# Optimization experiments

Hardware: AMD Instinct MI355X
Metric: run time of the kernel (lower is better)

## Reference

```python
import jax, jax.numpy as jnp
import numpy as np

IOU_THRESHOLD = 0.2


def setup_inputs() -> dict:
    key = jax.random.key(0)
    k1, k2, k3 = jax.random.split(key, 3)
    S, Q, X, Y, Z = 3, 64, 128, 128, 32
    C = 21  # 20 semantic classes + no-object
    voxel_logits = jax.random.normal(k1, (S, Q, X, Y, Z), dtype=jnp.float32)
    query_logits = jax.random.normal(k2, (S, 1, Q, C), dtype=jnp.float32)
    sem_prob_dense = jax.random.uniform(k3, (C, X, Y, Z), dtype=jnp.float32)
    return {"voxel_logits": voxel_logits, "query_logits": query_logits,
            "sem_prob_dense": sem_prob_dense}


def reference(voxel_logits, query_logits, sem_prob_dense):
    # voxel_logits: [S, Q, X, Y, Z], query_logits: [S, B, Q, C],
    # sem_prob_dense: [C_sem, X, Y, Z]
    S, Q, X, Y, Z = voxel_logits.shape
    N = X * Y * Z
    voxel_probs = jax.nn.sigmoid(voxel_logits).reshape(S, Q, N)   # MinkowskiSigmoid
    query_probs = jax.nn.softmax(query_logits, axis=-1)           # [S, B, Q, C]

    anchor_v = voxel_probs[0]   # [Q, N]
    anchor_q = query_probs[0]   # [B, Q, C]
    ious = []
    for i in range(1, S):  # small fixed loop over subnets
        aux_v = voxel_probs[i]
        # hard masks for IoU matching (find_matching_indices_v2)
        ma = (anchor_v > 0.5).astype(jnp.float32)  # [Q, N]
        mb = (aux_v > 0.5).astype(jnp.float32)     # [Q, N]
        inter = jnp.einsum('qn,pn->qp', ma, mb)    # [Q, Q]
        union = ma.sum(1)[:, None] + mb.sum(1)[None, :] - inter
        iou = inter / jnp.maximum(union, 1.0)
        aux_idx = jnp.argmax(iou, axis=1)          # best aux query per anchor
        iou_a = jnp.max(iou, axis=1)               # [Q]
        matched = iou_a > IOU_THRESHOLD
        # running-average merge of matched queries, weight i : 1
        merged_q = (anchor_q * i + query_probs[i][:, aux_idx, :]) / (i + 1)
        anchor_q = jnp.where(matched[None, :, None], merged_q, anchor_q)
        merged_v = (anchor_v * i + aux_v[aux_idx]) / (i + 1)
        anchor_v = jnp.where(matched[:, None], merged_v, anchor_v)
        ious.append(iou_a)

    iou_mean = jnp.stack(ious, axis=0).mean(0)     # [Q]
    keep = (iou_mean > IOU_THRESHOLD).astype(anchor_v.dtype)
    # mask out voxels whose ensemble semantic class is empty (class 0)
    sem_class = jnp.argmax(sem_prob_dense, axis=0)           # [X, Y, Z]
    occ = (sem_class != 0).astype(anchor_v.dtype).reshape(N)
    out = anchor_v * keep[:, None] * occ[None, :]
    return out.reshape(Q, X, Y, Z)
```

## Files before the change

### kernel.cpp

```cpp
#include <hip/hip_runtime.h>
#include <hip/hip_fp16.h>

#define NVOX 524288
#define NV4  131072
#define WPR  8192
#define QN   64
#define SN   3
#define CN   21

typedef unsigned long long u64;
typedef float vfloat4 __attribute__((ext_vector_type(4)));

struct __align__(8) half4 { __half2 lo, hi; };

__device__ __forceinline__ float fast_sigmoid(float x) {
    return __builtin_amdgcn_rcpf(1.0f + __expf(-x));
}

__device__ __forceinline__ void nt_store4(float4 v, float4* p) {
    vfloat4 nv = {v.x, v.y, v.z, v.w};
    __builtin_nontemporal_store(nv, (vfloat4*)p);
}

__global__ __launch_bounds__(256) void mask_rowsum_kernel(
    const float4* __restrict__ logits4, u64* __restrict__ B,
    unsigned int* __restrict__ part) {
    int r = blockIdx.x >> 3, c = blockIdx.x & 7;
    int tid = threadIdx.x, lane = tid & 63, wave = tid >> 6;
    const float4* row = logits4 + (size_t)r * NV4;
    int base = c * (NV4 / 8);
    int pcnt = 0;
#pragma unroll 2
    for (int it = 0; it < 64; ++it) {
        int idx = base + it * 256 + tid;
        float4 v = row[idx];
        int nib = (v.x > 0.f ? 1 : 0) | (v.y > 0.f ? 2 : 0) |
                  (v.z > 0.f ? 4 : 0) | (v.w > 0.f ? 8 : 0);
        pcnt += __popc(nib);
        u64 b0 = __ballot(nib & 1);
        u64 b1 = __ballot(nib & 2);
        u64 b2 = __ballot(nib & 4);
        u64 b3 = __ballot(nib & 8);
        if (lane == 0) {
            int seg = idx >> 6;
            ulonglong2* dst = (ulonglong2*)&B[(size_t)r * WPR + (size_t)seg * 4];
            dst[0] = make_ulonglong2(b0, b1);
            dst[1] = make_ulonglong2(b2, b3);
        }
    }
    for (int off = 32; off; off >>= 1) pcnt += __shfl_down(pcnt, off);
    __shared__ int red[4];
    if (lane == 0) red[wave] = pcnt;
    __syncthreads();
    if (tid == 0) part[blockIdx.x] = (unsigned)(red[0] + red[1] + red[2] + red[3]);
}

__global__ __launch_bounds__(256) void inter_kernel(
    const u64* __restrict__ Ba, const u64* __restrict__ Bb,
    unsigned int* __restrict__ inter) {
    int q0 = blockIdx.y * 4, p0 = blockIdx.x * 4;
    int tid = threadIdx.x;
    const ulonglong2* A2 = (const ulonglong2*)Ba;
    const ulonglong2* B2 = (const ulonglong2*)Bb;
    int acc[4][4] = {};
    for (int w = tid; w < WPR / 2; w += 256) {
        ulonglong2 a[4], b[4];
#pragma unroll
        for (int i = 0; i < 4; ++i) a[i] = A2[(size_t)(q0 + i) * (WPR / 2) + w];
#pragma unroll
        for (int j = 0; j < 4; ++j) b[j] = B2[(size_t)(p0 + j) * (WPR / 2) + w];
#pragma unroll
        for (int i = 0; i < 4; ++i)
#pragma unroll
            for (int j = 0; j < 4; ++j)
                acc[i][j] += __popcll(a[i].x & b[j].x) + __popcll(a[i].y & b[j].y);
    }
    __shared__ int red[16][4];
    int lane = tid & 63, wave = tid >> 6;
#pragma unroll
    for (int i = 0; i < 4; ++i)
#pragma unroll
        for (int j = 0; j < 4; ++j) {
            int v = acc[i][j];
            for (int off = 32; off; off >>= 1) v += __shfl_down(v, off);
            if (lane == 0) red[i * 4 + j][wave] = v;
        }
    __syncthreads();
    if (tid < 16) {
        int s = red[tid][0] + red[tid][1] + red[tid][2] + red[tid][3];
        inter[(q0 + (tid >> 2)) * QN + (p0 + (tid & 3))] = (unsigned)s;
    }
}

__global__ void finalize_kernel(
    const unsigned int* __restrict__ inter,
    const unsigned int* __restrict__ pa,
    const unsigned int* __restrict__ pa_alt, const int* __restrict__ sel,
    const unsigned int* __restrict__ pb,
    int* __restrict__ idx, int* __restrict__ matched, float* __restrict__ iou_out,
    int stage2, const float* __restrict__ iou_prev, float* __restrict__ keep) {
    __shared__ float nb[QN];
    int q = threadIdx.x;
    unsigned sb = 0;
#pragma unroll
    for (int k = 0; k < 8; ++k) sb += pb[q * 8 + k];
    nb[q] = (float)sb;
    __syncthreads();
    const unsigned int* pr = (sel && !sel[q]) ? pa_alt : pa;
    unsigned sa = 0;
#pragma unroll
    for (int k = 0; k < 8; ++k) sa += pr[q * 8 + k];
    float na = (float)sa;
    float best = -1.0f;
    int bidx = 0;
    for (int p = 0; p < QN; ++p) {
        float fi = (float)inter[q * QN + p];
        float un = fmaxf(na + nb[p] - fi, 1.0f);
        float iou = fi / un;
        if (iou > best) { best = iou; bidx = p; }
    }
    idx[q] = bidx;
    iou_out[q] = best;
    matched[q] = (best > 0.2f) ? 1 : 0;
    if (stage2) keep[q] = (((iou_prev[q] + best) * 0.5f) > 0.2f) ? 1.0f : 0.0f;
}

__global__ __launch_bounds__(256) void mask2_kernel(
    const float4* __restrict__ logits4,
    const int* __restrict__ idx1, const int* __restrict__ m1,
    u64* __restrict__ B0p, unsigned int* __restrict__ partP,
    half4* __restrict__ a01w) {
    int q = blockIdx.x >> 3, c = blockIdx.x & 7;
    if (!m1[q]) return;
    int tid = threadIdx.x, lane = tid & 63, wave = tid >> 6;
    const float4* r0 = logits4 + (size_t)q * NV4;
    const float4* r1 = logits4 + (size_t)(QN + idx1[q]) * NV4;
    int base = c * (NV4 / 8);
    int pcnt = 0;
#pragma unroll 2
    for (int it = 0; it < 64; ++it) {
        int idx = base + it * 256 + tid;
        float4 a = r0[idx];
        float4 b = r1[idx];
        int nib = (a.x + b.x > 0.f ? 1 : 0) | (a.y + b.y > 0.f ? 2 : 0) |
                  (a.z + b.z > 0.f ? 4 : 0) | (a.w + b.w > 0.f ? 8 : 0);
        pcnt += __popc(nib);
        float v0 = (fast_sigmoid(a.x) + fast_sigmoid(b.x)) * 0.5f;
        float v1 = (fast_sigmoid(a.y) + fast_sigmoid(b.y)) * 0.5f;
        float v2 = (fast_sigmoid(a.z) + fast_sigmoid(b.z)) * 0.5f;
        float v3 = (fast_sigmoid(a.w) + fast_sigmoid(b.w)) * 0.5f;
        half4 h;
        h.lo = __floats2half2_rn(v0, v1);
        h.hi = __floats2half2_rn(v2, v3);
        a01w[(size_t)q * NV4 + idx] = h;
        u64 b0 = __ballot(nib & 1);
        u64 b1 = __ballot(nib & 2);
        u64 b2 = __ballot(nib & 4);
        u64 b3 = __ballot(nib & 8);
        if (lane == 0) {
            int seg = idx >> 6;
            ulonglong2* dst = (ulonglong2*)&B0p[(size_t)q * WPR + (size_t)seg * 4];
            dst[0] = make_ulonglong2(b0, b1);
            dst[1] = make_ulonglong2(b2, b3);
        }
    }
    for (int off = 32; off; off >>= 1) pcnt += __shfl_down(pcnt, off);
    __shared__ int red[4];
    if (lane == 0) red[wave] = pcnt;
    __syncthreads();
    if (tid == 0) partP[blockIdx.x] = (unsigned)(red[0] + red[1] + red[2] + red[3]);
}

__global__ __launch_bounds__(256) void final_kernel(
    const float4* __restrict__ logits4, const float4* __restrict__ sem4,
    const half4* __restrict__ a01,
    const int* __restrict__ m1_, const int* __restrict__ idx2_,
    const int* __restrict__ m2_, const float* __restrict__ keep_,
    float4* __restrict__ out4) {
    __shared__ int sm1[QN], sj2[QN], sm2[QN];
    __shared__ float sk[QN];
    __shared__ float4 sOcc[128];
    int tid = threadIdx.x;
    if (tid < QN) {
        sm1[tid] = m1_[tid]; sj2[tid] = idx2_[tid];
        sm2[tid] = m2_[tid]; sk[tid] = keep_[tid];
    }
    int colh = tid & 127, qh = tid >> 7;
    int n4 = blockIdx.x * 128 + colh;
    if (qh == 0) {
        float4 s0 = sem4[n4];
        float4 mx = sem4[NV4 + n4];
#pragma unroll
        for (int c = 2; c < CN; ++c) {
            float4 s = sem4[(size_t)c * NV4 + n4];
            mx.x = fmaxf(mx.x, s.x); mx.y = fmaxf(mx.y, s.y);
            mx.z = fmaxf(mx.z, s.z); mx.w = fmaxf(mx.w, s.w);
        }
        float4 o;
        o.x = (mx.x > s0.x) ? 1.f : 0.f; o.y = (mx.y > s0.y) ? 1.f : 0.f;
        o.z = (mx.z > s0.z) ? 1.f : 0.f; o.w = (mx.w > s0.w) ? 1.f : 0.f;
        sOcc[colh] = o;
    }
    __syncthreads();
    float4 oc = sOcc[colh];
#pragma unroll 4
    for (int qq = 0; qq < 32; ++qq) {
        int q = (qh << 5) + qq;
        float a0, a1, a2, a3;
        if (sm1[q]) {
            half4 h = a01[(size_t)q * NV4 + n4];
            float2 f0 = __half22float2(h.lo);
            float2 f1 = __half22float2(h.hi);
            a0 = f0.x; a1 = f0.y; a2 = f1.x; a3 = f1.y;
        } else {
            float4 l0 = logits4[(size_t)q * NV4 + n4];
            a0 = fast_sigmoid(l0.x); a1 = fast_sigmoid(l0.y);
            a2 = fast_sigmoid(l0.z); a3 = fast_sigmoid(l0.w);
        }
        if (sm2[q]) {
            float4 l2 = logits4[(size_t)(2 * QN + sj2[q]) * NV4 + n4];
            const float t = 1.0f / 3.0f;
            a0 = (a0 * 2.f + fast_sigmoid(l2.x)) * t;
            a1 = (a1 * 2.f + fast_sigmoid(l2.y)) * t;
            a2 = (a2 * 2.f + fast_sigmoid(l2.z)) * t;
            a3 = (a3 * 2.f + fast_sigmoid(l2.w)) * t;
        }
        float kq = sk[q];
        float4 o;
        o.x = a0 * kq * oc.x; o.y = a1 * kq * oc.y;
        o.z = a2 * kq * oc.z; o.w = a3 * kq * oc.w;
        nt_store4(o, &out4[(size_t)q * NV4 + n4]);
    }
}

extern "C" void kernel_launch(void* const* d_in, const int* in_sizes, int n_in,
                              void* d_out, int out_size, void* d_ws, size_t ws_size,
                              hipStream_t stream) {
    const float4* vox4 = (const float4*)d_in[0];
    const float4* sem4 = (const float4*)d_in[2];
    float4* out4 = (float4*)d_out;
    (void)in_sizes; (void)n_in; (void)out_size; (void)ws_size; (void)d_in;

    char* p = (char*)d_ws;
    u64* Ball = (u64*)p;
    u64* B0 = Ball;
    u64* B1 = Ball + 1 * (size_t)QN * WPR;
    u64* B2 = Ball + 2 * (size_t)QN * WPR;
    char* p2 = p + 3ull * QN * WPR * 8;
    half4* a01 = (half4*)p2;
    char* p3 = p2 + (size_t)QN * NV4 * sizeof(half4);
    unsigned int* inter1 = (unsigned int*)p3;
    unsigned int* inter2 = inter1 + QN * QN;
    unsigned int* partA  = inter2 + QN * QN;
    unsigned int* partP  = partA + 192 * 8;
    int* idx1 = (int*)(partP + 64 * 8);
    int* idx2 = idx1 + QN;
    int* m1   = idx2 + QN;
    int* m2   = m1 + QN;
    float* iou1 = (float*)(m2 + QN);
    float* iou2 = iou1 + QN;
    float* keep = iou2 + QN;

    mask_rowsum_kernel<<<SN * QN * 8, 256, 0, stream>>>(vox4, Ball, partA);

    inter_kernel<<<dim3(16, 16), 256, 0, stream>>>(B0, B1, inter1);
    finalize_kernel<<<1, 64, 0, stream>>>(inter1, partA, nullptr, nullptr,
                                          partA + QN * 8, idx1, m1, iou1,
                                          0, nullptr, nullptr);

    mask2_kernel<<<QN * 8, 256, 0, stream>>>(vox4, idx1, m1, B0, partP, a01);
    inter_kernel<<<dim3(16, 16), 256, 0, stream>>>(B0, B2, inter2);
    finalize_kernel<<<1, 64, 0, stream>>>(inter2, partP, partA, m1,
                                          partA + 2 * QN * 8, idx2, m2, iou2,
                                          1, iou1, keep);

    final_kernel<<<1024, 256, 0, stream>>>(
        vox4, sem4, a01, m1, idx2, m2, keep, out4);
}
```

Measured before the change: 736.0 us.

## Fuse finalize steps into intersection kernels via last-block atomics; merge mask2 with inter2

Both small single-block finalize kernels are folded into the preceding kernels using a last-block-done atomic counter pattern. The second-stage mask kernel now keeps its bit-words in shared memory and computes the intersection counts against the third subnet's masks directly, accumulating with global atomics. This removes three kernel launches and the write-then-reread of the merged masks. The cost is atomic contention on inter2, plus each block rereading all 64 rows of the third subnet's bit chunk.

```diff
diff --git a/kernel.cpp b/kernel.cpp
--- a/kernel.cpp
+++ b/kernel.cpp
@@ -7,6 +7,7 @@
 #define QN   64
 #define SN   3
 #define CN   21
+#define CHUNK_W 1024
 
 typedef unsigned long long u64;
 typedef float vfloat4 __attribute__((ext_vector_type(4)));
@@ -24,7 +25,12 @@
 
 __global__ __launch_bounds__(256) void mask_rowsum_kernel(
     const float4* __restrict__ logits4, u64* __restrict__ B,
-    unsigned int* __restrict__ part) {
+    unsigned int* __restrict__ part, unsigned int* __restrict__ ctrl,
+    unsigned int* __restrict__ inter2) {
+    if (blockIdx.x == 0) {
+        if (threadIdx.x < 2) ctrl[threadIdx.x] = 0u;
+        for (int i = threadIdx.x; i < QN * QN; i += 256) inter2[i] = 0u;
+    }
     int r = blockIdx.x >> 3, c = blockIdx.x & 7;
     int tid = threadIdx.x, lane = tid & 63, wave = tid >> 6;
     const float4* row = logits4 + (size_t)r * NV4;
@@ -55,9 +61,11 @@
     if (tid == 0) part[blockIdx.x] = (unsigned)(red[0] + red[1] + red[2] + red[3]);
 }
 
-__global__ __launch_bounds__(256) void inter_kernel(
+__global__ __launch_bounds__(256) void inter1_fin1_kernel(
     const u64* __restrict__ Ba, const u64* __restrict__ Bb,
-    unsigned int* __restrict__ inter) {
+    unsigned int* __restrict__ inter,
+    const unsigned int* __restrict__ partA, unsigned int* __restrict__ ctrl,
+    int* __restrict__ idx1, int* __restrict__ m1, float* __restrict__ iou1) {
     int q0 = blockIdx.y * 4, p0 = blockIdx.x * 4;
     int tid = threadIdx.x;
     const ulonglong2* A2 = (const ulonglong2*)Ba;
@@ -90,85 +98,135 @@
         int s = red[tid][0] + red[tid][1] + red[tid][2] + red[tid][3];
         inter[(q0 + (tid >> 2)) * QN + (p0 + (tid & 3))] = (unsigned)s;
     }
-}
-
-__global__ void finalize_kernel(
-    const unsigned int* __restrict__ inter,
-    const unsigned int* __restrict__ pa,
-    const unsigned int* __restrict__ pa_alt, const int* __restrict__ sel,
-    const unsigned int* __restrict__ pb,
-    int* __restrict__ idx, int* __restrict__ matched, float* __restrict__ iou_out,
-    int stage2, const float* __restrict__ iou_prev, float* __restrict__ keep) {
+    __threadfence();
+    __shared__ int isLast;
+    __syncthreads();
+    if (tid == 0) isLast = (atomicAdd(&ctrl[0], 1u) == 16u * 16u - 1u);
+    __syncthreads();
+    if (!isLast) return;
+    __threadfence();
     __shared__ float nb[QN];
-    int q = threadIdx.x;
-    unsigned sb = 0;
-#pragma unroll
-    for (int k = 0; k < 8; ++k) sb += pb[q * 8 + k];
-    nb[q] = (float)sb;
-    __syncthreads();
-    const unsigned int* pr = (sel && !sel[q]) ? pa_alt : pa;
-    unsigned sa = 0;
-#pragma unroll
-    for (int k = 0; k < 8; ++k) sa += pr[q * 8 + k];
-    float na = (float)sa;
-    float best = -1.0f;
-    int bidx = 0;
+    if (tid < QN) {
+        unsigned sb = 0;
+#pragma unroll
+        for (int k = 0; k < 8; ++k) sb += partA[QN * 8 + tid * 8 + k];
+        nb[tid] = (float)sb;
+    }
+    __syncthreads();
+    if (tid < QN) {
+        unsigned sa = 0;
+#pragma unroll
+        for (int k = 0; k < 8; ++k) sa += partA[tid * 8 + k];
+        float na = (float)sa;
+        float best = -1.0f;
+        int bidx = 0;
+        for (int p = 0; p < QN; ++p) {
+            float fi = (float)inter[tid * QN + p];
+            float un = fmaxf(na + nb[p] - fi, 1.0f);
+            float iou = fi / un;
+            if (iou > best) { best = iou; bidx = p; }
+        }
+        idx1[tid] = bidx;
+        iou1[tid] = best;
+        m1[tid] = (best > 0.2f) ? 1 : 0;
+    }
+}
+
+__global__ __launch_bounds__(256) void merged2_kernel(
+    const float4* __restrict__ logits4, const u64* __restrict__ B0,
+    const u64* __restrict__ B2r,
+    const int* __restrict__ idx1, const int* __restrict__ m1,
+    unsigned int* __restrict__ partP, half4* __restrict__ a01w,
+    unsigned int* __restrict__ inter2, unsigned int* __restrict__ ctrl,
+    const unsigned int* __restrict__ partA, const float* __restrict__ iou1,
+    int* __restrict__ idx2, int* __restrict__ m2, float* __restrict__ keep) {
+    __shared__ u64 words[CHUNK_W];
+    __shared__ int red[4];
+    int q = blockIdx.x >> 3, c = blockIdx.x & 7;
+    int tid = threadIdx.x, lane = tid & 63, wave = tid >> 6;
+    bool matched = (m1[q] != 0);
+    if (matched) {
+        const float4* r0 = logits4 + (size_t)q * NV4;
+        const float4* r1 = logits4 + (size_t)(QN + idx1[q]) * NV4;
+        int base = c * (NV4 / 8);
+        int pcnt = 0;
+#pragma unroll 2
+        for (int it = 0; it < 64; ++it) {
+            int idx = base + it * 256 + tid;
+            float4 a = r0[idx];
+            float4 b = r1[idx];
+            int nib = (a.x + b.x > 0.f ? 1 : 0) | (a.y + b.y > 0.f ? 2 : 0) |
+                      (a.z + b.z > 0.f ? 4 : 0) | (a.w + b.w > 0.f ? 8 : 0);
+            pcnt += __popc(nib);
+            float v0 = (fast_sigmoid(a.x) + fast_sigmoid(b.x)) * 0.5f;
+            float v1 = (fast_sigmoid(a.y) + fast_sigmoid(b.y)) * 0.5f;
+            float v2 = (fast_sigmoid(a.z) + fast_sigmoid(b.z)) * 0.5f;
+            float v3 = (fast_sigmoid(a.w) + fast_sigmoid(b.w)) * 0.5f;
+            half4 h;
+            h.lo = __floats2half2_rn(v0, v1);
+            h.hi = __floats2half2_rn(v2, v3);
+            a01w[(size_t)q * NV4 + idx] = h;
+            u64 b0 = __ballot(nib & 1);
+            u64 b1 = __ballot(nib & 2);
+            u64 b2 = __ballot(nib & 4);
+            u64 b3 = __ballot(nib & 8);
+            if (lane < 4) {
+                u64 sel = (lane == 0) ? b0 : (lane == 1) ? b1 : (lane == 2) ? b2 : b3;
+                words[it * 16 + wave * 4 + lane] = sel;
+            }
+        }
+        for (int off = 32; off; off >>= 1) pcnt += __shfl_down(pcnt, off);
+        if (lane == 0) red[wave] = pcnt;
+    } else {
+        const u64* src = B0 + (size_t)q * WPR + (size_t)c * CHUNK_W;
+        for (int t = tid; t < CHUNK_W; t += 256) words[t] = src[t];
+    }
+    __syncthreads();
+    if (matched && tid == 0)
+        partP[blockIdx.x] = (unsigned)(red[0] + red[1] + red[2] + red[3]);
+    u64 w0 = words[tid], w1 = words[tid + 256];
+    u64 w2 = words[tid + 512], w3 = words[tid + 768];
+    const u64* B2c = B2r + (size_t)c * CHUNK_W;
     for (int p = 0; p < QN; ++p) {
-        float fi = (float)inter[q * QN + p];
-        float un = fmaxf(na + nb[p] - fi, 1.0f);
-        float iou = fi / un;
-        if (iou > best) { best = iou; bidx = p; }
-    }
-    idx[q] = bidx;
-    iou_out[q] = best;
-    matched[q] = (best > 0.2f) ? 1 : 0;
-    if (stage2) keep[q] = (((iou_prev[q] + best) * 0.5f) > 0.2f) ? 1.0f : 0.0f;
-}
-
-__global__ __launch_bounds__(256) void mask2_kernel(
-    const float4* __restrict__ logits4,
-    const int* __restrict__ idx1, const int* __restrict__ m1,
-    u64* __restrict__ B0p, unsigned int* __restrict__ partP,
-    half4* __restrict__ a01w) {
-    int q = blockIdx.x >> 3, c = blockIdx.x & 7;
-    if (!m1[q]) return;
-    int tid = threadIdx.x, lane = tid & 63, wave = tid >> 6;
-    const float4* r0 = logits4 + (size_t)q * NV4;
-    const float4* r1 = logits4 + (size_t)(QN + idx1[q]) * NV4;
-    int base = c * (NV4 / 8);
-    int pcnt = 0;
-#pragma unroll 2
-    for (int it = 0; it < 64; ++it) {
-        int idx = base + it * 256 + tid;
-        float4 a = r0[idx];
-        float4 b = r1[idx];
-        int nib = (a.x + b.x > 0.f ? 1 : 0) | (a.y + b.y > 0.f ? 2 : 0) |
-                  (a.z + b.z > 0.f ? 4 : 0) | (a.w + b.w > 0.f ? 8 : 0);
-        pcnt += __popc(nib);
-        float v0 = (fast_sigmoid(a.x) + fast_sigmoid(b.x)) * 0.5f;
-        float v1 = (fast_sigmoid(a.y) + fast_sigmoid(b.y)) * 0.5f;
-        float v2 = (fast_sigmoid(a.z) + fast_sigmoid(b.z)) * 0.5f;
-        float v3 = (fast_sigmoid(a.w) + fast_sigmoid(b.w)) * 0.5f;
-        half4 h;
-        h.lo = __floats2half2_rn(v0, v1);
-        h.hi = __floats2half2_rn(v2, v3);
-        a01w[(size_t)q * NV4 + idx] = h;
-        u64 b0 = __ballot(nib & 1);
-        u64 b1 = __ballot(nib & 2);
-        u64 b2 = __ballot(nib & 4);
-        u64 b3 = __ballot(nib & 8);
-        if (lane == 0) {
-            int seg = idx >> 6;
-            ulonglong2* dst = (ulonglong2*)&B0p[(size_t)q * WPR + (size_t)seg * 4];
-            dst[0] = make_ulonglong2(b0, b1);
-            dst[1] = make_ulonglong2(b2, b3);
-        }
-    }
-    for (int off = 32; off; off >>= 1) pcnt += __shfl_down(pcnt, off);
-    __shared__ int red[4];
-    if (lane == 0) red[wave] = pcnt;
-    __syncthreads();
-    if (tid == 0) partP[blockIdx.x] = (unsigned)(red[0] + red[1] + red[2] + red[3]);
+        const u64* row = B2c + (size_t)p * WPR;
+        int acc = __popcll(w0 & row[tid]) + __popcll(w1 & row[tid + 256]) +
+                  __popcll(w2 & row[tid + 512]) + __popcll(w3 & row[tid + 768]);
+        for (int off = 32; off; off >>= 1) acc += __shfl_down(acc, off);
+        if (lane == 0) atomicAdd(&inter2[q * QN + p], (unsigned)acc);
+    }
+    __threadfence();
+    __shared__ int isLast;
+    __syncthreads();
+    if (tid == 0) isLast = (atomicAdd(&ctrl[1], 1u) == (unsigned)(QN * 8 - 1));
+    __syncthreads();
+    if (!isLast) return;
+    __threadfence();
+    __shared__ float nb[QN];
+    if (tid < QN) {
+        unsigned sb = 0;
+#pragma unroll
+        for (int k = 0; k < 8; ++k) sb += partA[2 * QN * 8 + tid * 8 + k];
+        nb[tid] = (float)sb;
+    }
+    __syncthreads();
+    if (tid < QN) {
+        const unsigned int* pr = m1[tid] ? (partP + tid * 8) : (partA + tid * 8);
+        unsigned sa = 0;
+#pragma unroll
+        for (int k = 0; k < 8; ++k) sa += pr[k];
+        float na = (float)sa;
+        float best = -1.0f;
+        int bidx = 0;
+        for (int p = 0; p < QN; ++p) {
+            float fi = (float)inter2[tid * QN + p];
+            float un = fmaxf(na + nb[p] - fi, 1.0f);
+            float iou = fi / un;
+            if (iou > best) { best = iou; bidx = p; }
+        }
+        idx2[tid] = bidx;
+        m2[tid] = (best > 0.2f) ? 1 : 0;
+        keep[tid] = (((iou1[tid] + best) * 0.5f) > 0.2f) ? 1.0f : 0.0f;
+    }
 }
 
 __global__ __launch_bounds__(256) void final_kernel(
@@ -239,7 +297,7 @@
     const float4* vox4 = (const float4*)d_in[0];
     const float4* sem4 = (const float4*)d_in[2];
     float4* out4 = (float4*)d_out;
-    (void)in_sizes; (void)n_in; (void)out_size; (void)ws_size; (void)d_in;
+    (void)in_sizes; (void)n_in; (void)out_size; (void)ws_size;
 
     char* p = (char*)d_ws;
     u64* Ball = (u64*)p;
@@ -258,22 +316,16 @@
     int* m1   = idx2 + QN;
     int* m2   = m1 + QN;
     float* iou1 = (float*)(m2 + QN);
-    float* iou2 = iou1 + QN;
-    float* keep = iou2 + QN;
-
-    mask_rowsum_kernel<<<SN * QN * 8, 256, 0, stream>>>(vox4, Ball, partA);
-
-    inter_kernel<<<dim3(16, 16), 256, 0, stream>>>(B0, B1, inter1);
-    finalize_kernel<<<1, 64, 0, stream>>>(inter1, partA, nullptr, nullptr,
-                                          partA + QN * 8, idx1, m1, iou1,
-                                          0, nullptr, nullptr);
-
-    mask2_kernel<<<QN * 8, 256, 0, stream>>>(vox4, idx1, m1, B0, partP, a01);
-    inter_kernel<<<dim3(16, 16), 256, 0, stream>>>(B0, B2, inter2);
-    finalize_kernel<<<1, 64, 0, stream>>>(inter2, partP, partA, m1,
-                                          partA + 2 * QN * 8, idx2, m2, iou2,
-                                          1, iou1, keep);
-
+    float* keep = iou1 + QN;
+    unsigned int* ctrl = (unsigned int*)(keep + QN);
+
+    mask_rowsum_kernel<<<SN * QN * 8, 256, 0, stream>>>(vox4, Ball, partA,
+                                                        ctrl, inter2);
+    inter1_fin1_kernel<<<dim3(16, 16), 256, 0, stream>>>(
+        B0, B1, inter1, partA, ctrl, idx1, m1, iou1);
+    merged2_kernel<<<QN * 8, 256, 0, stream>>>(
+        vox4, B0, B2, idx1, m1, partP, a01, inter2, ctrl, partA, iou1,
+        idx2, m2, keep);
     final_kernel<<<1024, 256, 0, stream>>>(
         vox4, sem4, a01, m1, idx2, m2, keep, out4);
 }
```

After: 846.9 us. 1.15x slower.
